# Performance work log

Measured on AMD Instinct MI355X. Metric: run time of the kernel, lower is better.

Reference implementation:

```python
import jax, jax.numpy as jnp
import numpy as np

NUM_NODES = 200000
MEM_DIM = 128
TIME_DIM = 100
EDGE_DIM = 128
MSG_DIM = 256
E = 65536


def setup_inputs() -> dict:
    key = jax.random.key(0)
    ks = jax.random.split(key, 12)
    basis_freq = jnp.asarray(1.0 / 10 ** np.linspace(0, 9, TIME_DIM), dtype=jnp.float32)
    return {
        "src": jax.random.randint(ks[0], (E,), 0, NUM_NODES),
        "dst": jax.random.randint(ks[1], (E,), 0, NUM_NODES),
        "ts": jax.random.uniform(ks[2], (E,), dtype=jnp.float32),
        "edge_feats": jax.random.normal(ks[3], (E, EDGE_DIM), dtype=jnp.float32),
        "memory": jax.random.normal(ks[4], (NUM_NODES, MEM_DIM), dtype=jnp.float32),
        "last_update_ts": jnp.zeros((NUM_NODES,), dtype=jnp.float32),
        "basis_freq": basis_freq,
        "phase": jnp.zeros((TIME_DIM,), dtype=jnp.float32),
        "W_msg": jax.random.normal(ks[5], (MSG_DIM, 2 * MEM_DIM + TIME_DIM + EDGE_DIM), dtype=jnp.float32) * 0.05,
        "b_msg": jnp.zeros((MSG_DIM,), dtype=jnp.float32),
        "W_ih": jax.random.normal(ks[6], (3 * MEM_DIM, MSG_DIM), dtype=jnp.float32) * 0.05,
        "W_hh": jax.random.normal(ks[7], (3 * MEM_DIM, MEM_DIM), dtype=jnp.float32) * 0.05,
        "b_ih": jnp.zeros((3 * MEM_DIM,), dtype=jnp.float32),
        "b_hh": jnp.zeros((3 * MEM_DIM,), dtype=jnp.float32),
    }


def _time_enc(dt, basis_freq, phase):
    # dt: [E,1] -> [E,TIME_DIM]
    return jnp.cos(dt * basis_freq[None, :] + phase[None, :])


def reference(src, dst, ts, edge_feats, memory, last_update_ts,
              basis_freq, phase, W_msg, b_msg, W_ih, W_hh, b_ih, b_hh):
    n = memory.shape[0]
    ts_col = ts[:, None]                               # [E,1]
    prev_src_mem = memory[src]                         # [E,D]
    prev_dst_mem = memory[dst]
    tenc_src = _time_enc(ts_col - last_update_ts[src][:, None], basis_freq, phase)
    tenc_dst = _time_enc(ts_col - last_update_ts[dst][:, None], basis_freq, phase)

    # message MLP (dropout = identity, eval mode)
    x_dst = jnp.concatenate([prev_src_mem, prev_dst_mem, tenc_dst, edge_feats], axis=1)
    x_src = jnp.concatenate([prev_dst_mem, prev_src_mem, tenc_src, edge_feats], axis=1)
    msg_dst = jax.nn.relu(x_dst @ W_msg.T + b_msg)     # [E,M]
    msg_src = jax.nn.relu(x_src @ W_msg.T + b_msg)

    all_nodes = jnp.concatenate([src, dst], axis=0)    # [2E]
    all_msgs = jnp.concatenate([msg_src, msg_dst], axis=0)  # [2E,M]

    # per-node mean aggregation via segment sums (vectorized unique-loop)
    msg_sum = jax.ops.segment_sum(all_msgs, all_nodes, num_segments=n)
    counts = jax.ops.segment_sum(jnp.ones_like(all_nodes, dtype=msg_sum.dtype),
                                 all_nodes, num_segments=n)
    agg = msg_sum / jnp.maximum(counts, 1.0)[:, None]  # [N,M]

    # GRU cell update (torch.nn.GRUCell semantics)
    gi = agg @ W_ih.T + b_ih                           # [N,3D]
    gh = memory @ W_hh.T + b_hh
    i_r, i_z, i_n = jnp.split(gi, 3, axis=1)
    h_r, h_z, h_n = jnp.split(gh, 3, axis=1)
    r = jax.nn.sigmoid(i_r + h_r)
    z = jax.nn.sigmoid(i_z + h_z)
    nn_ = jnp.tanh(i_n + r * h_n)
    h_new = (1.0 - z) * nn_ + z * memory

    updated = counts > 0
    new_memory = jnp.where(updated[:, None], h_new, memory)

    # last_update_ts scatter-amax
    ts_rep = jnp.concatenate([ts, ts], axis=0)
    max_ts = jnp.zeros((n,), dtype=last_update_ts.dtype).at[all_nodes].max(ts_rep)
    new_last_update_ts = jnp.maximum(last_update_ts, max_ts)
    return new_memory, new_last_update_ts
```

## Files before the change

### kernel.cpp

```cpp
#include <hip/hip_runtime.h>
#include <hip/hip_bf16.h>
#include <math.h>

#define NNODES 200000
#define EDGES  65536
#define NSIDES (2*EDGES)
#define MD 128
#define TD 100
#define EDIM 128
#define MSGD 256
#define KX 512
#define KG 384
#define NSCAN 782
#define GBLK 64

typedef __attribute__((ext_vector_type(8))) short bf16x8;
typedef __attribute__((ext_vector_type(4))) float f32x4;

#define O_COUNTS    0u
#define O_NUMUPD    800000u
#define O_BSUMC     800004u
#define O_BSUMF     803132u
#define O_UPDLIST   806272u
#define O_SEGSTART  1330592u
#define O_CNTLIST   1854912u
#define O_BMSG      2379200u
#define O_BG        2641344u
#define O_BH        2936256u
#define O_MSGBUF    2969088u
#define WS_NEEDED   (2969088ull + 67108864ull)

__device__ __forceinline__ short f2bf(float v) {
    unsigned x = __float_as_uint(v);
    unsigned r = (x + 0x7fffu + ((x >> 16) & 1u)) >> 16;
    return (short)r;
}
__device__ __forceinline__ float bflo(unsigned u) { return __uint_as_float(u << 16); }
__device__ __forceinline__ float bfhi(unsigned u) { return __uint_as_float(u & 0xffff0000u); }
__device__ __forceinline__ float bf2f(unsigned short u) {
    return __uint_as_float(((unsigned)u) << 16);
}
__device__ __forceinline__ f32x4 mfma16(bf16x8 a, bf16x8 b, f32x4 c) {
    return __builtin_amdgcn_mfma_f32_16x16x32_bf16(a, b, c, 0, 0, 0);
}

__global__ __launch_bounds__(256) void k_copy(const float* __restrict__ mem,
                                              const float* __restrict__ last,
                                              float* __restrict__ out) {
    const size_t n4m = (size_t)NNODES * MD / 4;
    const size_t n4t = NNODES / 4;
    const float4* m4 = (const float4*)mem;
    const float4* l4 = (const float4*)last;
    float4* o4  = (float4*)out;
    float4* ot4 = (float4*)(out + (size_t)NNODES * MD);
    size_t stride = (size_t)gridDim.x * blockDim.x;
    for (size_t i = blockIdx.x * (size_t)blockDim.x + threadIdx.x; i < n4m + n4t; i += stride) {
        if (i < n4m) o4[i] = m4[i];
        else ot4[i - n4m] = l4[i - n4m];
    }
}

__global__ __launch_bounds__(256) void k_pack(const float* __restrict__ wmsg,
                                              const float* __restrict__ wih,
                                              const float* __restrict__ whh,
                                              short* __restrict__ bmsgp,
                                              short* __restrict__ bgp,
                                              short* __restrict__ bhp) {
    const int NM = 16 * 16 * 64 * 8;
    const int NG = 12 * 24 * 64 * 8;
    const int NH = 4 * 8 * 64 * 8;
    int idx = blockIdx.x * 256 + threadIdx.x;
    if (idx < NM) {
        int j = idx & 7, l = (idx >> 3) & 63, nf = (idx >> 9) & 15, ks = idx >> 13;
        int n = nf * 16 + (l & 15);
        int k = ks * 32 + ((l >> 4) << 3) + j;
        bmsgp[idx] = f2bf(k < 484 ? wmsg[n * 484 + k] : 0.f);
    } else if (idx < NM + NG) {
        int i = idx - NM;
        int j = i & 7, l = (i >> 3) & 63, rest = i >> 9;
        int nf = rest % 24, ks = rest / 24;
        int n = nf * 16 + (l & 15);
        int k = ks * 32 + ((l >> 4) << 3) + j;
        float v = (k < 256) ? wih[n * 256 + k] : whh[n * 128 + (k - 256)];
        bgp[i] = f2bf(v);
    } else if (idx < NM + NG + NH) {
        int i = idx - NM - NG;
        int j = i & 7, l = (i >> 3) & 63, rest = i >> 9;
        int nf = rest & 7, ks = rest >> 3;
        int n = 256 + nf * 16 + (l & 15);
        int k = ks * 32 + ((l >> 4) << 3) + j;
        bhp[i] = f2bf(whh[n * 128 + k]);
    }
}

__global__ __launch_bounds__(256) void k_edges(const int* __restrict__ src, const int* __restrict__ dst,
                                               const float* __restrict__ ts,
                                               int* __restrict__ counts, float* __restrict__ out_ts) {
    int e = blockIdx.x * blockDim.x + threadIdx.x;
    if (e >= EDGES) return;
    int s = src[e], d = dst[e];
    unsigned tb = __float_as_uint(ts[e]);
    atomicAdd(&counts[s], 1);
    atomicAdd(&counts[d], 1);
    atomicMax((unsigned*)&out_ts[s], tb);
    atomicMax((unsigned*)&out_ts[d], tb);
}

__global__ __launch_bounds__(256) void k_scan1(const int* __restrict__ counts,
                                               int* __restrict__ bsumC, int* __restrict__ bsumF) {
    __shared__ int sC[256], sF[256];
    int t = threadIdx.x, i = blockIdx.x * 256 + t;
    int c = (i < NNODES) ? counts[i] : 0;
    sC[t] = c; sF[t] = (c > 0) ? 1 : 0;
    __syncthreads();
    for (int off = 128; off > 0; off >>= 1) {
        if (t < off) { sC[t] += sC[t + off]; sF[t] += sF[t + off]; }
        __syncthreads();
    }
    if (t == 0) { bsumC[blockIdx.x] = sC[0]; bsumF[blockIdx.x] = sF[0]; }
}

__global__ __launch_bounds__(1024) void k_scan2(int* __restrict__ bsumC, int* __restrict__ bsumF,
                                                int* __restrict__ numupd) {
    __shared__ int sC[1024], sF[1024];
    int t = threadIdx.x;
    int c = (t < NSCAN) ? bsumC[t] : 0;
    int f = (t < NSCAN) ? bsumF[t] : 0;
    sC[t] = c; sF[t] = f;
    __syncthreads();
    for (int off = 1; off < 1024; off <<= 1) {
        int vc = (t >= off) ? sC[t - off] : 0;
        int vf = (t >= off) ? sF[t - off] : 0;
        __syncthreads();
        sC[t] += vc; sF[t] += vf;
        __syncthreads();
    }
    if (t < NSCAN) { bsumC[t] = sC[t] - c; bsumF[t] = sF[t] - f; }
    if (t == 0) numupd[0] = sF[1023];
}

__global__ __launch_bounds__(256) void k_scan3(int* __restrict__ counts,
                                               const int* __restrict__ bsumC, const int* __restrict__ bsumF,
                                               int* __restrict__ updlist, int* __restrict__ segstart,
                                               int* __restrict__ cntlist, const int* __restrict__ numupd) {
    __shared__ int sC[256], sF[256];
    int t = threadIdx.x, b = blockIdx.x, i = b * 256 + t;
    int c = (i < NNODES) ? counts[i] : 0;
    int fl = (c > 0) ? 1 : 0;
    sC[t] = c; sF[t] = fl;
    __syncthreads();
    for (int off = 1; off < 256; off <<= 1) {
        int vc = (t >= off) ? sC[t - off] : 0;
        int vf = (t >= off) ? sF[t - off] : 0;
        __syncthreads();
        sC[t] += vc; sF[t] += vf;
        __syncthreads();
    }
    if (i < NNODES) {
        int segC = bsumC[b] + sC[t] - c;
        int rank = bsumF[b] + sF[t] - fl;
        if (fl) {
            updlist[rank]  = i;
            segstart[rank] = segC;
            cntlist[rank]  = c;
        }
        counts[i] = segC;
        if (i == NNODES - 1) segstart[numupd[0]] = segC + c;
    }
}

__global__ __launch_bounds__(512) void k_msg(const int* __restrict__ src, const int* __restrict__ dst,
                                             const float* __restrict__ ts, const float* __restrict__ ef,
                                             const float* __restrict__ mem, const float* __restrict__ last,
                                             const float* __restrict__ bfq, const float* __restrict__ ph,
                                             const short* __restrict__ Bp, const float* __restrict__ bmsg,
                                             int* __restrict__ cursor, unsigned short* __restrict__ msgbuf) {
    __shared__ short As[64 * KX];
    __shared__ int srcS[32], dstS[32], posS[64];
    __shared__ float dtS[64];
    const int t = threadIdx.x;
    const int e0 = blockIdx.x * 32;

    if (t < 64) {
        int el = t >> 1, which = t & 1;
        int e = e0 + el;
        int s = src[e], d = dst[e];
        int self = which ? d : s;
        if (which == 0) { srcS[el] = s; dstS[el] = d; }
        dtS[t]  = ts[e] - last[self];
        posS[t] = atomicAdd(&cursor[self], 1);
    }
    __syncthreads();

    const int c4 = t & 31;
    const int rg = t >> 5;
    #pragma unroll
    for (int i = 0; i < 4; ++i) {
        int nr = rg + i * 16;
        int el = nr >> 1, which = nr & 1;
        int node = which ? dstS[el] : srcS[el];
        float4 v = *(const float4*)&mem[(size_t)node * MD + c4 * 4];
        short4 b = make_short4(f2bf(v.x), f2bf(v.y), f2bf(v.z), f2bf(v.w));
        int rA = 2 * el, rB = 2 * el + 1;
        int swA = (rA & 7) << 3, swB = (rB & 7) << 3;
        int c16 = c4 * 4;
        if (which == 0) {
            *(short4*)&As[rA * KX + ((128 + c16) ^ swA)] = b;
            *(short4*)&As[rB * KX + ((0   + c16) ^ swB)] = b;
        } else {
            *(short4*)&As[rA * KX + ((0   + c16) ^ swA)] = b;
            *(short4*)&As[rB * KX + ((128 + c16) ^ swB)] = b;
        }
    }
    #pragma unroll
    for (int i = 0; i < 2; ++i) {
        int el = rg + i * 16;
        float4 v = *(const float4*)&ef[(size_t)(e0 + el) * EDIM + c4 * 4];
        short4 b = make_short4(f2bf(v.x), f2bf(v.y), f2bf(v.z), f2bf(v.w));
        int k = 356 + c4 * 4;
        int rA = 2 * el, rB = 2 * el + 1;
        *(short4*)&As[rA * KX + (k ^ ((rA & 7) << 3))] = b;
        *(short4*)&As[rB * KX + (k ^ ((rB & 7) << 3))] = b;
    }
    {
        int s = t & 63, jg = t >> 6;
        float dt = dtS[s];
        int sw = (s & 7) << 3;
        int j1 = min(jg * 13 + 13, TD);
        for (int j = jg * 13; j < j1; ++j) {
            float v = __cosf(fmaf(dt, bfq[j], ph[j]));
            As[s * KX + ((256 + j) ^ sw)] = f2bf(v);
        }
    }
    if (t < 448) {
        int s = t / 7, p = t % 7;
        int sw = (s & 7) << 3;
        int k = 484 + p * 4;
        *(short4*)&As[s * KX + (k ^ sw)] = make_short4(0, 0, 0, 0);
    }
    __syncthreads();

    const int w = t >> 6, l = t & 63, lc = l & 15, lq = l >> 4;
    f32x4 acc[4][2];
    #pragma unroll
    for (int i = 0; i < 4; ++i)
        #pragma unroll
        for (int j = 0; j < 2; ++j) acc[i][j] = (f32x4){0.f, 0.f, 0.f, 0.f};

    const int rsw = (lc & 7) << 3;
    for (int ks = 0; ks < 16; ++ks) {
        bf16x8 a[4];
        #pragma unroll
        for (int rt = 0; rt < 4; ++rt)
            a[rt] = *(const bf16x8*)&As[(rt * 16 + lc) * KX + ((ks * 32 + (lq << 3)) ^ rsw)];
        #pragma unroll
        for (int f = 0; f < 2; ++f) {
            bf16x8 b = *(const bf16x8*)(Bp + (size_t)(ks * 16 + w * 2 + f) * 512 + l * 8);
            #pragma unroll
            for (int rt = 0; rt < 4; ++rt)
                acc[rt][f] = mfma16(a[rt], b, acc[rt][f]);
        }
    }

    float bb[2];
    #pragma unroll
    for (int f = 0; f < 2; ++f) bb[f] = bmsg[w * 32 + f * 16 + lc];
    #pragma unroll
    for (int rt = 0; rt < 4; ++rt) {
        #pragma unroll
        for (int jj = 0; jj < 4; ++jj) {
            int srow = rt * 16 + lq * 4 + jj;
            unsigned short* orow = msgbuf + (size_t)posS[srow] * MSGD;
            #pragma unroll
            for (int f = 0; f < 2; ++f) {
                int c = w * 32 + f * 16 + lc;
                float v = fmaxf(acc[rt][f][jj] + bb[f], 0.f);
                orow[c] = (unsigned short)f2bf(v);
            }
        }
    }
}

__global__ __launch_bounds__(512) void k_gru(const int* __restrict__ updlist, const int* __restrict__ segstart,
                                             const int* __restrict__ cntlist, const int* __restrict__ numupd,
                                             const unsigned short* __restrict__ msgbuf,
                                             const float* __restrict__ mem,
                                             const short* __restrict__ Bg, const short* __restrict__ Bh,
                                             const float* __restrict__ bih, const float* __restrict__ bhh,
                                             float* __restrict__ outmem) {
    __shared__ short Ag[GBLK * KG];
    __shared__ int sb[GBLK + 1];
    __shared__ int nodesh[GBLK];
    __shared__ float invh[GBLK];
    const int nu = *numupd;
    const int slot0 = blockIdx.x * GBLK;
    if (slot0 >= nu) return;
    const int t = threadIdx.x;
    if (t < GBLK + 1) sb[t] = segstart[min(slot0 + t, nu)];
    if (t < GBLK) {
        int slot = slot0 + t;
        if (slot < nu) { nodesh[t] = updlist[slot]; invh[t] = 1.f / (float)cntlist[slot]; }
        else           { nodesh[t] = -1;            invh[t] = 0.f; }
    }
    __syncthreads();

    {
        const int c4 = t & 31, rg = t >> 5;
        #pragma unroll
        for (int i = 0; i < 4; ++i) {
            int s = rg + i * 16;
            int node = nodesh[s];
            float4 v = make_float4(0.f, 0.f, 0.f, 0.f);
            if (node >= 0) v = *(const float4*)&mem[(size_t)node * MD + c4 * 4];
            int sw = (s & 7) << 3;
            *(short4*)&Ag[s * KG + ((256 + c4 * 4) ^ sw)] =
                make_short4(f2bf(v.x), f2bf(v.y), f2bf(v.z), f2bf(v.w));
        }
    }
    {
        const int g = t >> 3, q = t & 7;
        float acc[32];
        #pragma unroll
        for (int m = 0; m < 32; ++m) acc[m] = 0.f;
        const int j0 = sb[g], j1 = sb[g + 1];
        for (int j = j0; j < j1; ++j) {
            const unsigned short* rp = msgbuf + (size_t)j * MSGD + q * 32;
            #pragma unroll
            for (int h = 0; h < 4; ++h) {
                uint4 u = *(const uint4*)(rp + h * 8);
                acc[h*8+0] += bflo(u.x); acc[h*8+1] += bfhi(u.x);
                acc[h*8+2] += bflo(u.y); acc[h*8+3] += bfhi(u.y);
                acc[h*8+4] += bflo(u.z); acc[h*8+5] += bfhi(u.z);
                acc[h*8+6] += bflo(u.w); acc[h*8+7] += bfhi(u.w);
            }
        }
        const float inv = invh[g];
        const int sw = (g & 7) << 3;
        #pragma unroll
        for (int h = 0; h < 4; ++h) {
            bf16x8 o;
            #pragma unroll
            for (int m = 0; m < 8; ++m) o[m] = f2bf(acc[h * 8 + m] * inv);
            *(bf16x8*)&Ag[g * KG + ((q * 32 + h * 8) ^ sw)] = o;
        }
    }
    __syncthreads();

    const int w = t >> 6, l = t & 63, lc = l & 15, lq = l >> 4;
    f32x4 accS[4][3], accH[4];
    #pragma unroll
    for (int rt = 0; rt < 4; ++rt) {
        #pragma unroll
        for (int g = 0; g < 3; ++g) accS[rt][g] = (f32x4){0.f, 0.f, 0.f, 0.f};
        accH[rt] = (f32x4){0.f, 0.f, 0.f, 0.f};
    }

    const int rsw = (lc & 7) << 3;
    for (int ks = 0; ks < 12; ++ks) {
        bf16x8 a[4];
        #pragma unroll
        for (int rt = 0; rt < 4; ++rt)
            a[rt] = *(const bf16x8*)&Ag[(rt * 16 + lc) * KG + ((ks * 32 + (lq << 3)) ^ rsw)];
        #pragma unroll
        for (int g = 0; g < 3; ++g) {
            bf16x8 b = *(const bf16x8*)(Bg + (size_t)(ks * 24 + g * 8 + w) * 512 + l * 8);
            #pragma unroll
            for (int rt = 0; rt < 4; ++rt)
                accS[rt][g] = mfma16(a[rt], b, accS[rt][g]);
        }
        if (ks >= 8) {
            bf16x8 b = *(const bf16x8*)(Bh + (size_t)((ks - 8) * 8 + w) * 512 + l * 8);
            #pragma unroll
            for (int rt = 0; rt < 4; ++rt)
                accH[rt] = mfma16(a[rt], b, accH[rt]);
        }
    }

    {
        int d = w * 16 + lc;
        float br  = bih[d] + bhh[d];
        float bz  = bih[MD + d] + bhh[MD + d];
        float bin = bih[2 * MD + d];
        float bhn = bhh[2 * MD + d];
        #pragma unroll
        for (int rt = 0; rt < 4; ++rt) {
            #pragma unroll
            for (int jj = 0; jj < 4; ++jj) {
                int srow = rt * 16 + lq * 4 + jj;
                int node = nodesh[srow];
                if (node < 0) continue;
                float S_r = accS[rt][0][jj] + br;
                float S_z = accS[rt][1][jj] + bz;
                float hn  = accH[rt][jj] + bhn;
                float in_ = accS[rt][2][jj] - accH[rt][jj] + bin;
                float rr = 1.f / (1.f + __expf(-S_r));
                float zz = 1.f / (1.f + __expf(-S_z));
                float x  = fminf(fmaxf(in_ + rr * hn, -15.f), 15.f);
                float ex = __expf(-2.f * x);
                float nn = (1.f - ex) / (1.f + ex);
                int sw = (srow & 7) << 3;
                float mv = bf2f((unsigned short)Ag[srow * KG + ((256 + d) ^ sw)]);
                outmem[(size_t)node * MD + d] = (1.f - zz) * nn + zz * mv;
            }
        }
    }
}

extern "C" void kernel_launch(void* const* d_in, const int* in_sizes, int n_in,
                              void* d_out, int out_size, void* d_ws, size_t ws_size,
                              hipStream_t stream) {
    const int*   src  = (const int*)d_in[0];
    const int*   dst  = (const int*)d_in[1];
    const float* ts   = (const float*)d_in[2];
    const float* ef   = (const float*)d_in[3];
    const float* mem  = (const float*)d_in[4];
    const float* last = (const float*)d_in[5];
    const float* bfq  = (const float*)d_in[6];
    const float* ph   = (const float*)d_in[7];
    const float* wmsg = (const float*)d_in[8];
    const float* bmsg = (const float*)d_in[9];
    const float* wih  = (const float*)d_in[10];
    const float* whh  = (const float*)d_in[11];
    const float* bih  = (const float*)d_in[12];
    const float* bhh  = (const float*)d_in[13];
    float* out = (float*)d_out;
    char* ws = (char*)d_ws;

    if (ws_size < WS_NEEDED) return;

    int* counts   = (int*)(ws + O_COUNTS);
    int* numupd   = (int*)(ws + O_NUMUPD);
    int* bsumC    = (int*)(ws + O_BSUMC);
    int* bsumF    = (int*)(ws + O_BSUMF);
    int* updlist  = (int*)(ws + O_UPDLIST);
    int* segstart = (int*)(ws + O_SEGSTART);
    int* cntlist  = (int*)(ws + O_CNTLIST);
    short* bmsgp  = (short*)(ws + O_BMSG);
    short* bgp    = (short*)(ws + O_BG);
    short* bhp    = (short*)(ws + O_BH);
    unsigned short* msgbuf = (unsigned short*)(ws + O_MSGBUF);
    float* out_ts = out + (size_t)NNODES * MD;

    hipMemsetAsync(ws + O_COUNTS, 0, 800004, stream);

    k_copy <<<4096, 256, 0, stream>>>(mem, last, out);
    k_pack <<<1152, 256, 0, stream>>>(wmsg, wih, whh, bmsgp, bgp, bhp);
    k_edges<<<EDGES / 256, 256, 0, stream>>>(src, dst, ts, counts, out_ts);
    k_scan1<<<NSCAN, 256, 0, stream>>>(counts, bsumC, bsumF);
    k_scan2<<<1, 1024, 0, stream>>>(bsumC, bsumF, numupd);
    k_scan3<<<NSCAN, 256, 0, stream>>>(counts, bsumC, bsumF, updlist, segstart, cntlist, numupd);
    k_msg  <<<EDGES / 32, 512, 0, stream>>>(src, dst, ts, ef, mem, last, bfq, ph, bmsgp, bmsg, counts, msgbuf);
    k_gru  <<<NSIDES / GBLK, 512, 0, stream>>>(updlist, segstart, cntlist, numupd, msgbuf, mem, bgp, bhp, bih, bhh, out);
}
```

Measured before the change: 203.2 us.

## Copy only non-updated memory rows and halve LDS tiles in msg and GRU kernels

The full memory-to-output copy becomes a timestamp copy plus a masked memory copy. The masked copy runs after the scan and skips rows that the GRU kernel will overwrite, using a new per-node update flag. The message and GRU kernels now reuse a half-size LDS tile in two phases, reloading the second half of the K dimension after the first MFMA pass. This halves shared memory per block so more blocks can be resident, at the cost of extra barriers. bf16 packing also switches to a paired-pack helper.

```diff
diff --git a/kernel.cpp b/kernel.cpp
--- a/kernel.cpp
+++ b/kernel.cpp
@@ -9,8 +9,6 @@
 #define TD 100
 #define EDIM 128
 #define MSGD 256
-#define KX 512
-#define KG 384
 #define NSCAN 782
 #define GBLK 64
 
@@ -28,13 +26,21 @@
 #define O_BG        2641344u
 #define O_BH        2936256u
 #define O_MSGBUF    2969088u
-#define WS_NEEDED   (2969088ull + 67108864ull)
+#define O_UPDFLAG   (2969088u + 67108864u)
+#define WS_NEEDED   (2969088ull + 67108864ull + 200000ull)
 
 __device__ __forceinline__ short f2bf(float v) {
     unsigned x = __float_as_uint(v);
     unsigned r = (x + 0x7fffu + ((x >> 16) & 1u)) >> 16;
     return (short)r;
 }
+__device__ __forceinline__ unsigned pk2bf(float a, float b) {
+    unsigned xa = __float_as_uint(a);
+    unsigned xb = __float_as_uint(b);
+    unsigned ra = (xa + 0x7fffu + ((xa >> 16) & 1u)) >> 16;
+    unsigned rb = (xb + 0x7fffu + ((xb >> 16) & 1u)) & 0xffff0000u;
+    return ra | rb;
+}
 __device__ __forceinline__ float bflo(unsigned u) { return __uint_as_float(u << 16); }
 __device__ __forceinline__ float bfhi(unsigned u) { return __uint_as_float(u & 0xffff0000u); }
 __device__ __forceinline__ float bf2f(unsigned short u) {
@@ -44,20 +50,20 @@
     return __builtin_amdgcn_mfma_f32_16x16x32_bf16(a, b, c, 0, 0, 0);
 }
 
-__global__ __launch_bounds__(256) void k_copy(const float* __restrict__ mem,
-                                              const float* __restrict__ last,
-                                              float* __restrict__ out) {
-    const size_t n4m = (size_t)NNODES * MD / 4;
-    const size_t n4t = NNODES / 4;
-    const float4* m4 = (const float4*)mem;
-    const float4* l4 = (const float4*)last;
-    float4* o4  = (float4*)out;
-    float4* ot4 = (float4*)(out + (size_t)NNODES * MD);
-    size_t stride = (size_t)gridDim.x * blockDim.x;
-    for (size_t i = blockIdx.x * (size_t)blockDim.x + threadIdx.x; i < n4m + n4t; i += stride) {
-        if (i < n4m) o4[i] = m4[i];
-        else ot4[i - n4m] = l4[i - n4m];
-    }
+__global__ __launch_bounds__(256) void k_copy_ts(const float* __restrict__ last,
+                                                 float* __restrict__ out_ts) {
+    int i = blockIdx.x * 256 + threadIdx.x;
+    if (i < NNODES / 4) ((float4*)out_ts)[i] = ((const float4*)last)[i];
+}
+
+__global__ __launch_bounds__(256) void k_copy_mem(const float* __restrict__ mem,
+                                                  const unsigned char* __restrict__ updflag,
+                                                  float* __restrict__ out) {
+    size_t idx = (size_t)blockIdx.x * 256 + threadIdx.x;
+    if (idx >= (size_t)NNODES * 32) return;
+    int node = (int)(idx >> 5);
+    if (updflag[node]) return;
+    ((float4*)out)[idx] = ((const float4*)mem)[idx];
 }
 
 __global__ __launch_bounds__(256) void k_pack(const float* __restrict__ wmsg,
@@ -142,7 +148,8 @@
 __global__ __launch_bounds__(256) void k_scan3(int* __restrict__ counts,
                                                const int* __restrict__ bsumC, const int* __restrict__ bsumF,
                                                int* __restrict__ updlist, int* __restrict__ segstart,
-                                               int* __restrict__ cntlist, const int* __restrict__ numupd) {
+                                               int* __restrict__ cntlist, const int* __restrict__ numupd,
+                                               unsigned char* __restrict__ updflag) {
     __shared__ int sC[256], sF[256];
     int t = threadIdx.x, b = blockIdx.x, i = b * 256 + t;
     int c = (i < NNODES) ? counts[i] : 0;
@@ -164,6 +171,7 @@
             segstart[rank] = segC;
             cntlist[rank]  = c;
         }
+        updflag[i] = (unsigned char)fl;
         counts[i] = segC;
         if (i == NNODES - 1) segstart[numupd[0]] = segC + c;
     }
@@ -175,7 +183,7 @@
                                              const float* __restrict__ bfq, const float* __restrict__ ph,
                                              const short* __restrict__ Bp, const float* __restrict__ bmsg,
                                              int* __restrict__ cursor, unsigned short* __restrict__ msgbuf) {
-    __shared__ short As[64 * KX];
+    __shared__ short As[64 * 256];
     __shared__ int srcS[32], dstS[32], posS[64];
     __shared__ float dtS[64];
     const int t = threadIdx.x;
@@ -200,59 +208,78 @@
         int el = nr >> 1, which = nr & 1;
         int node = which ? dstS[el] : srcS[el];
         float4 v = *(const float4*)&mem[(size_t)node * MD + c4 * 4];
-        short4 b = make_short4(f2bf(v.x), f2bf(v.y), f2bf(v.z), f2bf(v.w));
+        uint2 b = make_uint2(pk2bf(v.x, v.y), pk2bf(v.z, v.w));
         int rA = 2 * el, rB = 2 * el + 1;
         int swA = (rA & 7) << 3, swB = (rB & 7) << 3;
         int c16 = c4 * 4;
         if (which == 0) {
-            *(short4*)&As[rA * KX + ((128 + c16) ^ swA)] = b;
-            *(short4*)&As[rB * KX + ((0   + c16) ^ swB)] = b;
+            *(uint2*)&As[rA * 256 + ((128 + c16) ^ swA)] = b;
+            *(uint2*)&As[rB * 256 + ((0   + c16) ^ swB)] = b;
         } else {
-            *(short4*)&As[rA * KX + ((0   + c16) ^ swA)] = b;
-            *(short4*)&As[rB * KX + ((128 + c16) ^ swB)] = b;
-        }
-    }
-    #pragma unroll
-    for (int i = 0; i < 2; ++i) {
-        int el = rg + i * 16;
-        float4 v = *(const float4*)&ef[(size_t)(e0 + el) * EDIM + c4 * 4];
-        short4 b = make_short4(f2bf(v.x), f2bf(v.y), f2bf(v.z), f2bf(v.w));
-        int k = 356 + c4 * 4;
-        int rA = 2 * el, rB = 2 * el + 1;
-        *(short4*)&As[rA * KX + (k ^ ((rA & 7) << 3))] = b;
-        *(short4*)&As[rB * KX + (k ^ ((rB & 7) << 3))] = b;
-    }
+            *(uint2*)&As[rA * 256 + ((0   + c16) ^ swA)] = b;
+            *(uint2*)&As[rB * 256 + ((128 + c16) ^ swB)] = b;
+        }
+    }
+    __syncthreads();
+
+    const int w = t >> 6, l = t & 63, lc = l & 15, lq = l >> 4;
+    f32x4 acc[4][2];
+    #pragma unroll
+    for (int i = 0; i < 4; ++i)
+        #pragma unroll
+        for (int j = 0; j < 2; ++j) acc[i][j] = (f32x4){0.f, 0.f, 0.f, 0.f};
+
+    const int rsw = (lc & 7) << 3;
+    #pragma unroll 2
+    for (int ks = 0; ks < 8; ++ks) {
+        bf16x8 a[4];
+        #pragma unroll
+        for (int rt = 0; rt < 4; ++rt)
+            a[rt] = *(const bf16x8*)&As[(rt * 16 + lc) * 256 + ((ks * 32 + (lq << 3)) ^ rsw)];
+        #pragma unroll
+        for (int f = 0; f < 2; ++f) {
+            bf16x8 b = *(const bf16x8*)(Bp + (size_t)(ks * 16 + w * 2 + f) * 512 + l * 8);
+            #pragma unroll
+            for (int rt = 0; rt < 4; ++rt)
+                acc[rt][f] = mfma16(a[rt], b, acc[rt][f]);
+        }
+    }
+    __syncthreads();
+
     {
         int s = t & 63, jg = t >> 6;
         float dt = dtS[s];
         int sw = (s & 7) << 3;
-        int j1 = min(jg * 13 + 13, TD);
-        for (int j = jg * 13; j < j1; ++j) {
-            float v = __cosf(fmaf(dt, bfq[j], ph[j]));
-            As[s * KX + ((256 + j) ^ sw)] = f2bf(v);
-        }
+        int p1 = min(jg * 7 + 7, 50);
+        for (int p = jg * 7; p < p1; ++p) {
+            float v0 = __cosf(fmaf(dt, bfq[2 * p],     ph[2 * p]));
+            float v1 = __cosf(fmaf(dt, bfq[2 * p + 1], ph[2 * p + 1]));
+            *(unsigned*)&As[s * 256 + ((2 * p) ^ sw)] = pk2bf(v0, v1);
+        }
+    }
+    #pragma unroll
+    for (int i = 0; i < 2; ++i) {
+        int el = rg + i * 16;
+        float4 v = *(const float4*)&ef[(size_t)(e0 + el) * EDIM + c4 * 4];
+        uint2 b = make_uint2(pk2bf(v.x, v.y), pk2bf(v.z, v.w));
+        int k = 100 + c4 * 4;
+        int rA = 2 * el, rB = 2 * el + 1;
+        *(uint2*)&As[rA * 256 + (k ^ ((rA & 7) << 3))] = b;
+        *(uint2*)&As[rB * 256 + (k ^ ((rB & 7) << 3))] = b;
     }
     if (t < 448) {
         int s = t / 7, p = t % 7;
         int sw = (s & 7) << 3;
-        int k = 484 + p * 4;
-        *(short4*)&As[s * KX + (k ^ sw)] = make_short4(0, 0, 0, 0);
-    }
-    __syncthreads();
-
-    const int w = t >> 6, l = t & 63, lc = l & 15, lq = l >> 4;
-    f32x4 acc[4][2];
-    #pragma unroll
-    for (int i = 0; i < 4; ++i)
-        #pragma unroll
-        for (int j = 0; j < 2; ++j) acc[i][j] = (f32x4){0.f, 0.f, 0.f, 0.f};
-
-    const int rsw = (lc & 7) << 3;
-    for (int ks = 0; ks < 16; ++ks) {
+        *(uint2*)&As[s * 256 + ((228 + p * 4) ^ sw)] = make_uint2(0u, 0u);
+    }
+    __syncthreads();
+
+    #pragma unroll 2
+    for (int ks = 8; ks < 16; ++ks) {
         bf16x8 a[4];
         #pragma unroll
         for (int rt = 0; rt < 4; ++rt)
-            a[rt] = *(const bf16x8*)&As[(rt * 16 + lc) * KX + ((ks * 32 + (lq << 3)) ^ rsw)];
+            a[rt] = *(const bf16x8*)&As[(rt * 16 + lc) * 256 + (((ks - 8) * 32 + (lq << 3)) ^ rsw)];
         #pragma unroll
         for (int f = 0; f < 2; ++f) {
             bf16x8 b = *(const bf16x8*)(Bp + (size_t)(ks * 16 + w * 2 + f) * 512 + l * 8);
@@ -288,7 +315,7 @@
                                              const short* __restrict__ Bg, const short* __restrict__ Bh,
                                              const float* __restrict__ bih, const float* __restrict__ bhh,
                                              float* __restrict__ outmem) {
-    __shared__ short Ag[GBLK * KG];
+    __shared__ short Ag[64 * 256];
     __shared__ int sb[GBLK + 1];
     __shared__ int nodesh[GBLK];
     __shared__ float invh[GBLK];
@@ -305,19 +332,6 @@
     __syncthreads();
 
     {
-        const int c4 = t & 31, rg = t >> 5;
-        #pragma unroll
-        for (int i = 0; i < 4; ++i) {
-            int s = rg + i * 16;
-            int node = nodesh[s];
-            float4 v = make_float4(0.f, 0.f, 0.f, 0.f);
-            if (node >= 0) v = *(const float4*)&mem[(size_t)node * MD + c4 * 4];
-            int sw = (s & 7) << 3;
-            *(short4*)&Ag[s * KG + ((256 + c4 * 4) ^ sw)] =
-                make_short4(f2bf(v.x), f2bf(v.y), f2bf(v.z), f2bf(v.w));
-        }
-    }
-    {
         const int g = t >> 3, q = t & 7;
         float acc[32];
         #pragma unroll
@@ -338,10 +352,12 @@
         const int sw = (g & 7) << 3;
         #pragma unroll
         for (int h = 0; h < 4; ++h) {
-            bf16x8 o;
-            #pragma unroll
-            for (int m = 0; m < 8; ++m) o[m] = f2bf(acc[h * 8 + m] * inv);
-            *(bf16x8*)&Ag[g * KG + ((q * 32 + h * 8) ^ sw)] = o;
+            uint4 o;
+            o.x = pk2bf(acc[h*8+0] * inv, acc[h*8+1] * inv);
+            o.y = pk2bf(acc[h*8+2] * inv, acc[h*8+3] * inv);
+            o.z = pk2bf(acc[h*8+4] * inv, acc[h*8+5] * inv);
+            o.w = pk2bf(acc[h*8+6] * inv, acc[h*8+7] * inv);
+            *(uint4*)&Ag[g * 256 + ((q * 32 + h * 8) ^ sw)] = o;
         }
     }
     __syncthreads();
@@ -354,13 +370,13 @@
         for (int g = 0; g < 3; ++g) accS[rt][g] = (f32x4){0.f, 0.f, 0.f, 0.f};
         accH[rt] = (f32x4){0.f, 0.f, 0.f, 0.f};
     }
-
     const int rsw = (lc & 7) << 3;
-    for (int ks = 0; ks < 12; ++ks) {
+    #pragma unroll 2
+    for (int ks = 0; ks < 8; ++ks) {
         bf16x8 a[4];
         #pragma unroll
         for (int rt = 0; rt < 4; ++rt)
-            a[rt] = *(const bf16x8*)&Ag[(rt * 16 + lc) * KG + ((ks * 32 + (lq << 3)) ^ rsw)];
+            a[rt] = *(const bf16x8*)&Ag[(rt * 16 + lc) * 256 + ((ks * 32 + (lq << 3)) ^ rsw)];
         #pragma unroll
         for (int g = 0; g < 3; ++g) {
             bf16x8 b = *(const bf16x8*)(Bg + (size_t)(ks * 24 + g * 8 + w) * 512 + l * 8);
@@ -368,12 +384,41 @@
             for (int rt = 0; rt < 4; ++rt)
                 accS[rt][g] = mfma16(a[rt], b, accS[rt][g]);
         }
-        if (ks >= 8) {
-            bf16x8 b = *(const bf16x8*)(Bh + (size_t)((ks - 8) * 8 + w) * 512 + l * 8);
+    }
+    __syncthreads();
+
+    {
+        const int c4 = t & 31, rg = t >> 5;
+        #pragma unroll
+        for (int i = 0; i < 4; ++i) {
+            int s = rg + i * 16;
+            int node = nodesh[s];
+            float4 v = make_float4(0.f, 0.f, 0.f, 0.f);
+            if (node >= 0) v = *(const float4*)&mem[(size_t)node * MD + c4 * 4];
+            int sw = (s & 7) << 3;
+            *(uint2*)&Ag[s * 128 + ((c4 * 4) ^ sw)] =
+                make_uint2(pk2bf(v.x, v.y), pk2bf(v.z, v.w));
+        }
+    }
+    __syncthreads();
+
+    #pragma unroll
+    for (int ks = 8; ks < 12; ++ks) {
+        bf16x8 a[4];
+        #pragma unroll
+        for (int rt = 0; rt < 4; ++rt)
+            a[rt] = *(const bf16x8*)&Ag[(rt * 16 + lc) * 128 + (((ks - 8) * 32 + (lq << 3)) ^ rsw)];
+        #pragma unroll
+        for (int g = 0; g < 3; ++g) {
+            bf16x8 b = *(const bf16x8*)(Bg + (size_t)(ks * 24 + g * 8 + w) * 512 + l * 8);
             #pragma unroll
             for (int rt = 0; rt < 4; ++rt)
-                accH[rt] = mfma16(a[rt], b, accH[rt]);
-        }
+                accS[rt][g] = mfma16(a[rt], b, accS[rt][g]);
+        }
+        bf16x8 bh = *(const bf16x8*)(Bh + (size_t)((ks - 8) * 8 + w) * 512 + l * 8);
+        #pragma unroll
+        for (int rt = 0; rt < 4; ++rt)
+            accH[rt] = mfma16(a[rt], bh, accH[rt]);
     }
 
     {
@@ -399,7 +444,7 @@
                 float ex = __expf(-2.f * x);
                 float nn = (1.f - ex) / (1.f + ex);
                 int sw = (srow & 7) << 3;
-                float mv = bf2f((unsigned short)Ag[srow * KG + ((256 + d) ^ sw)]);
+                float mv = bf2f((unsigned short)Ag[srow * 128 + (d ^ sw)]);
                 outmem[(size_t)node * MD + d] = (1.f - zz) * nn + zz * mv;
             }
         }
@@ -439,16 +484,18 @@
     short* bgp    = (short*)(ws + O_BG);
     short* bhp    = (short*)(ws + O_BH);
     unsigned short* msgbuf = (unsigned short*)(ws + O_MSGBUF);
+    unsigned char*  updflag = (unsigned char*)(ws + O_UPDFLAG);
     float* out_ts = out + (size_t)NNODES * MD;
 
     hipMemsetAsync(ws + O_COUNTS, 0, 800004, stream);
 
-    k_copy <<<4096, 256, 0, stream>>>(mem, last, out);
+    k_copy_ts<<<(NNODES / 4 + 255) / 256, 256, 0, stream>>>(last, out_ts);
     k_pack <<<1152, 256, 0, stream>>>(wmsg, wih, whh, bmsgp, bgp, bhp);
     k_edges<<<EDGES / 256, 256, 0, stream>>>(src, dst, ts, counts, out_ts);
     k_scan1<<<NSCAN, 256, 0, stream>>>(counts, bsumC, bsumF);
     k_scan2<<<1, 1024, 0, stream>>>(bsumC, bsumF, numupd);
-    k_scan3<<<NSCAN, 256, 0, stream>>>(counts, bsumC, bsumF, updlist, segstart, cntlist, numupd);
+    k_scan3<<<NSCAN, 256, 0, stream>>>(counts, bsumC, bsumF, updlist, segstart, cntlist, numupd, updflag);
+    k_copy_mem<<<(NNODES * 32 + 255) / 256, 256, 0, stream>>>(mem, updflag, out);
     k_msg  <<<EDGES / 32, 512, 0, stream>>>(src, dst, ts, ef, mem, last, bfq, ph, bmsgp, bmsg, counts, msgbuf);
     k_gru  <<<NSIDES / GBLK, 512, 0, stream>>>(updlist, segstart, cntlist, numupd, msgbuf, mem, bgp, bhp, bih, bhh, out);
 }
```

Result: slower. 225.2 us (+10.9%).
